# Kernel optimization log

Measured on AMD Instinct MI355X. Metric: run time of the kernel, lower is better.

## Reference

```python
import jax, jax.numpy as jnp
import numpy as np

E = 800000
N = 50000
D = 128
SLOPE = 0.2


def setup_inputs() -> dict:
    key = jax.random.key(0)
    ks = jax.random.split(key, 8)
    M = jax.random.normal(ks[0], (E, D), dtype=jnp.float32)
    dest = jax.random.randint(ks[1], (E,), 0, N, dtype=jnp.int32)
    rev_index = jax.random.randint(ks[2], (E,), 0, E, dtype=jnp.int32)
    s = 1.0 / np.sqrt(D)
    W0 = jax.random.uniform(ks[3], (D, D), jnp.float32, -s, s)
    b0 = jax.random.uniform(ks[4], (D,), jnp.float32, -s, s)
    W1 = jax.random.uniform(ks[5], (D, D), jnp.float32, -s, s)
    b1 = jax.random.uniform(ks[6], (D,), jnp.float32, -s, s)
    sa = 1.0 / np.sqrt(D)
    a_w = jax.random.uniform(ks[7], (1, D), jnp.float32, -sa, sa)
    a_b = jnp.zeros((1,), jnp.float32)
    return {"M": M, "dest": dest, "rev_index": rev_index, "dim_size": N,
            "W0": W0, "b0": b0, "W1": W1, "b1": b1, "a_w": a_w, "a_b": a_b}


def reference(M, dest, rev_index, dim_size, W0, b0, W1, b1, a_w, a_b):
    # Z = LeakyReLU(W_0(M) + W_1(M[rev_index]))  -> [E, D]
    Z = jax.nn.leaky_relu(M @ W0.T + b0 + M[rev_index] @ W1.T + b1, negative_slope=SLOPE)
    # scores = a(Z) -> [E, 1]; segment softmax over dest
    s = (Z @ a_w.T + a_b)[:, 0]  # [E]
    smax = jax.ops.segment_max(s, dest, num_segments=dim_size)  # [N]
    e = jnp.exp(s - smax[dest])
    denom = jax.ops.segment_sum(e, dest, num_segments=dim_size)  # [N]
    alpha = (e / denom[dest])[:, None]  # [E, 1]
    out = jax.ops.segment_sum(alpha * M, dest, num_segments=dim_size)  # [N, D]
    return out, alpha
```

## Files before the change

kernel.cpp:

```cpp
#include <hip/hip_runtime.h>
#include <hip/hip_bf16.h>


#define SLOPE 0.2f
constexpr int E = 800000;
constexpr int N = 50000;
constexpr int D = 128;
constexpr int TILE_E = 64;
constexpr int NTILES = E / TILE_E;
constexpr int LDA = 264;
constexpr int MAXDEG = 64;

typedef __attribute__((ext_vector_type(8))) short bf16x8;
typedef __attribute__((ext_vector_type(4))) short short4v;
typedef __attribute__((ext_vector_type(4))) float f32x4;

__device__ __forceinline__ short f2bf(float f) {
    unsigned u = __float_as_uint(f);
    u = (u + 0x7fffu + ((u >> 16) & 1u)) >> 16;
    return (short)u;
}

__global__ void convert_w(const float* __restrict__ W0, const float* __restrict__ W1,
                          short* __restrict__ Wbf) {
    int i = blockIdx.x * blockDim.x + threadIdx.x;
    if (i >= D * 256) return;
    int d = i >> 8, k = i & 255;
    float v = (k < 128) ? W0[d * 128 + k] : W1[d * 128 + (k - 128)];
    Wbf[i] = f2bf(v);
}

__global__ void bucket_build(const int* __restrict__ dest, int* __restrict__ cnt,
                             int* __restrict__ bucket) {
    int e = blockIdx.x * blockDim.x + threadIdx.x;
    if (e >= E) return;
    int n = dest[e];
    int pos = atomicAdd(&cnt[n], 1);
    if (pos < MAXDEG) bucket[n * MAXDEG + pos] = e;
}

__global__ __launch_bounds__(512) void score_kernel(
    const float* __restrict__ M, const int* __restrict__ dest,
    const int* __restrict__ rev, const short* __restrict__ Wbf,
    const float* __restrict__ b0, const float* __restrict__ b1,
    const float* __restrict__ a_w, const float* __restrict__ a_b,
    float* __restrict__ pbuf, float* __restrict__ denom)
{
    __shared__ short Alds[TILE_E * LDA];
    __shared__ float red[4][TILE_E];

    const int t = threadIdx.x;
    const int w = t >> 6;
    const int lane = t & 63;
    const int lo = lane & 15, hi = lane >> 4;
    const int er = (w & 1) * 32;
    const int dr = (w >> 1) * 32;

    bf16x8 b[2][8];
#pragma unroll
    for (int j = 0; j < 2; ++j) {
        int d = dr + j * 16 + lo;
#pragma unroll
        for (int ks = 0; ks < 8; ++ks)
            b[j][ks] = *(const bf16x8*)(Wbf + d * 256 + ks * 32 + hi * 8);
    }
    float bs[2], aw[2];
#pragma unroll
    for (int j = 0; j < 2; ++j) {
        int d = dr + j * 16 + lo;
        bs[j] = b0[d] + b1[d];
        aw[j] = a_w[d];
    }
    const float ab = a_b[0];

    const int c  = t & 31;
    const int r0 = t >> 5;

    for (int tile = blockIdx.x; tile < NTILES; tile += gridDim.x) {
        const int ebase = tile * TILE_E;
        __syncthreads();

#pragma unroll
        for (int pp = 0; pp < 2; ++pp) {
            float4 vs[2], vr[2];
            int rv[2];
#pragma unroll
            for (int q = 0; q < 2; ++q)
                rv[q] = rev[ebase + r0 + (pp * 2 + q) * 16];
#pragma unroll
            for (int q = 0; q < 2; ++q)
                vs[q] = ((const float4*)(M + (size_t)(ebase + r0 + (pp * 2 + q) * 16) * D))[c];
#pragma unroll
            for (int q = 0; q < 2; ++q)
                vr[q] = ((const float4*)(M + (size_t)rv[q] * D))[c];
#pragma unroll
            for (int q = 0; q < 2; ++q) {
                int r = r0 + (pp * 2 + q) * 16;
                short4v s0 = { f2bf(vs[q].x), f2bf(vs[q].y), f2bf(vs[q].z), f2bf(vs[q].w) };
                *(short4v*)(Alds + r * LDA + c * 4) = s0;
                short4v s1 = { f2bf(vr[q].x), f2bf(vr[q].y), f2bf(vr[q].z), f2bf(vr[q].w) };
                *(short4v*)(Alds + r * LDA + 128 + c * 4) = s1;
            }
        }
        __syncthreads();

        f32x4 zero = {0.f, 0.f, 0.f, 0.f};
        f32x4 acc[2][2];
#pragma unroll
        for (int i = 0; i < 2; ++i)
#pragma unroll
            for (int j = 0; j < 2; ++j) acc[i][j] = zero;

#pragma unroll
        for (int ks = 0; ks < 8; ++ks) {
            bf16x8 a[2];
#pragma unroll
            for (int i = 0; i < 2; ++i)
                a[i] = *(const bf16x8*)(Alds + (er + i * 16 + lo) * LDA + ks * 32 + hi * 8);
#pragma unroll
            for (int i = 0; i < 2; ++i)
#pragma unroll
                for (int j = 0; j < 2; ++j)
                    acc[i][j] = __builtin_amdgcn_mfma_f32_16x16x32_bf16(a[i], b[j][ks], acc[i][j], 0, 0, 0);
        }

#pragma unroll
        for (int i = 0; i < 2; ++i) {
#pragma unroll
            for (int r = 0; r < 4; ++r) {
                float v = 0.f;
#pragma unroll
                for (int j = 0; j < 2; ++j) {
                    float x = acc[i][j][r] + bs[j];
                    x = (x > 0.f) ? x : SLOPE * x;
                    v += aw[j] * x;
                }
                v += __shfl_xor(v, 1);
                v += __shfl_xor(v, 2);
                v += __shfl_xor(v, 4);
                v += __shfl_xor(v, 8);
                if (lo == 0) red[w >> 1][er + i * 16 + hi * 4 + r] = v;
            }
        }
        __syncthreads();

        if (t < TILE_E) {
            float s = red[0][t] + red[1][t] + red[2][t] + red[3][t] + ab;
            float p = __expf(s);
            pbuf[ebase + t] = p;
            atomicAdd(&denom[dest[ebase + t]], p);
        }
    }
}

__global__ void norm_kernel(const int* __restrict__ dest, const float* __restrict__ denom,
                            float* __restrict__ alpha) {
    int e = blockIdx.x * blockDim.x + threadIdx.x;
    if (e < E) alpha[e] = alpha[e] / denom[dest[e]];
}

__global__ __launch_bounds__(256) void gather_kernel(
    const float* __restrict__ M, const float* __restrict__ alpha,
    const int* __restrict__ cnt, const int* __restrict__ bucket,
    float* __restrict__ out)
{
    const int n = blockIdx.x * 4 + (threadIdx.x >> 6);
    const int lane = threadIdx.x & 63;
    int c = cnt[n];
    c = (c > MAXDEG) ? MAXDEG : c;
    int e = 0; float a = 0.f;
    if (lane < c) {
        e = bucket[n * MAXDEG + lane];
        a = alpha[e];
    }
    float2 acc = {0.f, 0.f};
    for (int i = 0; i < c; ++i) {
        int   ei = __shfl(e, i);
        float ai = __shfl(a, i);
        float2 v = ((const float2*)(M + (size_t)ei * D))[lane];
        acc.x += ai * v.x;
        acc.y += ai * v.y;
    }
    ((float2*)(out + (size_t)n * D))[lane] = acc;
}

extern "C" void kernel_launch(void* const* d_in, const int* in_sizes, int n_in,
                              void* d_out, int out_size, void* d_ws, size_t ws_size,
                              hipStream_t stream) {
    const float* M   = (const float*)d_in[0];
    const int*   dst = (const int*)d_in[1];
    const int*   rev = (const int*)d_in[2];
    const float* W0  = (const float*)d_in[4];
    const float* b0  = (const float*)d_in[5];
    const float* W1  = (const float*)d_in[6];
    const float* b1  = (const float*)d_in[7];
    const float* a_w = (const float*)d_in[8];
    const float* a_b = (const float*)d_in[9];

    float* out   = (float*)d_out;
    float* alpha = out + (size_t)N * D;

    float* denom  = (float*)d_ws;
    short* Wbf    = (short*)(denom + N);
    int*   cnt    = (int*)(Wbf + D * 256);
    int*   bucket = cnt + N;

    hipMemsetAsync(denom, 0, (size_t)N * sizeof(float), stream);
    hipMemsetAsync(cnt, 0, (size_t)N * sizeof(int), stream);

    convert_w<<<128, 256, 0, stream>>>(W0, W1, Wbf);
    bucket_build<<<(E + 255) / 256, 256, 0, stream>>>(dst, cnt, bucket);
    score_kernel<<<512, 512, 0, stream>>>(M, dst, rev, Wbf, b0, b1, a_w, a_b, alpha, denom);
    norm_kernel<<<(E + 255) / 256, 256, 0, stream>>>(dst, denom, alpha);
    gather_kernel<<<N / 4, 256, 0, stream>>>(M, alpha, cnt, bucket, out);
}
```

Baseline: 766.3 us.

## Pre-convert M to bf16 and stream tiles into LDS via direct global loads

Adds a pass that converts M to a bf16 copy once. The score kernel then loads that copy straight into a swizzled LDS layout with global_load_lds, and the gather kernel also reads the bf16 copy. The normalisation kernel is folded into the gather, which now writes alpha itself. The intent is to shrink the memory traffic of the later passes and drop one launch, at the cost of an extra full read-and-write pass over M. The output aggregation also loses precision because it now sums bf16 values of M.

```diff
diff --git a/kernel.cpp b/kernel.cpp
--- a/kernel.cpp
+++ b/kernel.cpp
@@ -8,26 +8,38 @@
 constexpr int D = 128;
 constexpr int TILE_E = 64;
 constexpr int NTILES = E / TILE_E;
-constexpr int LDA = 264;
 constexpr int MAXDEG = 64;
 
 typedef __attribute__((ext_vector_type(8))) short bf16x8;
-typedef __attribute__((ext_vector_type(4))) short short4v;
+typedef __attribute__((ext_vector_type(8))) unsigned short u16x8;
 typedef __attribute__((ext_vector_type(4))) float f32x4;
 
-__device__ __forceinline__ short f2bf(float f) {
+__device__ __forceinline__ unsigned short f2bf(float f) {
     unsigned u = __float_as_uint(f);
     u = (u + 0x7fffu + ((u >> 16) & 1u)) >> 16;
-    return (short)u;
+    return (unsigned short)u;
 }
 
 __global__ void convert_w(const float* __restrict__ W0, const float* __restrict__ W1,
-                          short* __restrict__ Wbf) {
+                          unsigned short* __restrict__ Wbf) {
     int i = blockIdx.x * blockDim.x + threadIdx.x;
     if (i >= D * 256) return;
     int d = i >> 8, k = i & 255;
     float v = (k < 128) ? W0[d * 128 + k] : W1[d * 128 + (k - 128)];
     Wbf[i] = f2bf(v);
+}
+
+__global__ void convert_m(const float* __restrict__ M, unsigned short* __restrict__ Mbf) {
+    const size_t nchunk = (size_t)E * D / 8;
+    const size_t stride = (size_t)gridDim.x * blockDim.x;
+    for (size_t i = (size_t)blockIdx.x * blockDim.x + threadIdx.x; i < nchunk; i += stride) {
+        float4 v0 = ((const float4*)M)[i * 2];
+        float4 v1 = ((const float4*)M)[i * 2 + 1];
+        u16x8 u;
+        u[0] = f2bf(v0.x); u[1] = f2bf(v0.y); u[2] = f2bf(v0.z); u[3] = f2bf(v0.w);
+        u[4] = f2bf(v1.x); u[5] = f2bf(v1.y); u[6] = f2bf(v1.z); u[7] = f2bf(v1.w);
+        ((u16x8*)Mbf)[i] = u;
+    }
 }
 
 __global__ void bucket_build(const int* __restrict__ dest, int* __restrict__ cnt,
@@ -39,14 +51,14 @@
     if (pos < MAXDEG) bucket[n * MAXDEG + pos] = e;
 }
 
-__global__ __launch_bounds__(512) void score_kernel(
-    const float* __restrict__ M, const int* __restrict__ dest,
-    const int* __restrict__ rev, const short* __restrict__ Wbf,
+__global__ __launch_bounds__(512, 4) void score_kernel(
+    const unsigned short* __restrict__ Mbf, const int* __restrict__ dest,
+    const int* __restrict__ rev, const unsigned short* __restrict__ Wbf,
     const float* __restrict__ b0, const float* __restrict__ b1,
     const float* __restrict__ a_w, const float* __restrict__ a_b,
     float* __restrict__ pbuf, float* __restrict__ denom)
 {
-    __shared__ short Alds[TILE_E * LDA];
+    __shared__ unsigned short Alds[TILE_E * 256];
     __shared__ float red[4][TILE_E];
 
     const int t = threadIdx.x;
@@ -73,34 +85,29 @@
     }
     const float ab = a_b[0];
 
-    const int c  = t & 31;
-    const int r0 = t >> 5;
+    const int rbase = w * 8;
+    const int rsub = lane >> 5;
+    const int pc = lane & 31;
 
     for (int tile = blockIdx.x; tile < NTILES; tile += gridDim.x) {
         const int ebase = tile * TILE_E;
         __syncthreads();
 
-#pragma unroll
-        for (int pp = 0; pp < 2; ++pp) {
-            float4 vs[2], vr[2];
-            int rv[2];
-#pragma unroll
-            for (int q = 0; q < 2; ++q)
-                rv[q] = rev[ebase + r0 + (pp * 2 + q) * 16];
-#pragma unroll
-            for (int q = 0; q < 2; ++q)
-                vs[q] = ((const float4*)(M + (size_t)(ebase + r0 + (pp * 2 + q) * 16) * D))[c];
-#pragma unroll
-            for (int q = 0; q < 2; ++q)
-                vr[q] = ((const float4*)(M + (size_t)rv[q] * D))[c];
-#pragma unroll
-            for (int q = 0; q < 2; ++q) {
-                int r = r0 + (pp * 2 + q) * 16;
-                short4v s0 = { f2bf(vs[q].x), f2bf(vs[q].y), f2bf(vs[q].z), f2bf(vs[q].w) };
-                *(short4v*)(Alds + r * LDA + c * 4) = s0;
-                short4v s1 = { f2bf(vr[q].x), f2bf(vr[q].y), f2bf(vr[q].z), f2bf(vr[q].w) };
-                *(short4v*)(Alds + r * LDA + 128 + c * 4) = s1;
-            }
+        int revr[4];
+#pragma unroll
+        for (int k = 0; k < 4; ++k)
+            revr[k] = rev[ebase + rbase + 2 * k + rsub];
+#pragma unroll
+        for (int k = 0; k < 4; ++k) {
+            int r = rbase + 2 * k + rsub;
+            int cc = pc ^ (r & 7);
+            const unsigned short* g = (cc < 16)
+                ? Mbf + (size_t)(ebase + r) * 128 + cc * 8
+                : Mbf + (size_t)revr[k] * 128 + (cc - 16) * 8;
+            __builtin_amdgcn_global_load_lds(
+                (const __attribute__((address_space(1))) void*)g,
+                (__attribute__((address_space(3))) void*)(&Alds[(rbase + 2 * k) * 256]),
+                16, 0, 0);
         }
         __syncthreads();
 
@@ -115,8 +122,11 @@
         for (int ks = 0; ks < 8; ++ks) {
             bf16x8 a[2];
 #pragma unroll
-            for (int i = 0; i < 2; ++i)
-                a[i] = *(const bf16x8*)(Alds + (er + i * 16 + lo) * LDA + ks * 32 + hi * 8);
+            for (int i = 0; i < 2; ++i) {
+                int r = er + i * 16 + lo;
+                int pcx = (ks * 4 + hi) ^ (r & 7);
+                a[i] = *(const bf16x8*)(&Alds[r * 256 + pcx * 8]);
+            }
 #pragma unroll
             for (int i = 0; i < 2; ++i)
 #pragma unroll
@@ -153,33 +163,32 @@
     }
 }
 
-__global__ void norm_kernel(const int* __restrict__ dest, const float* __restrict__ denom,
-                            float* __restrict__ alpha) {
-    int e = blockIdx.x * blockDim.x + threadIdx.x;
-    if (e < E) alpha[e] = alpha[e] / denom[dest[e]];
-}
-
 __global__ __launch_bounds__(256) void gather_kernel(
-    const float* __restrict__ M, const float* __restrict__ alpha,
-    const int* __restrict__ cnt, const int* __restrict__ bucket,
-    float* __restrict__ out)
+    const unsigned short* __restrict__ Mbf, const float* __restrict__ p,
+    const float* __restrict__ denom, const int* __restrict__ cnt,
+    const int* __restrict__ bucket, float* __restrict__ out,
+    float* __restrict__ alpha_out)
 {
     const int n = blockIdx.x * 4 + (threadIdx.x >> 6);
     const int lane = threadIdx.x & 63;
     int c = cnt[n];
     c = (c > MAXDEG) ? MAXDEG : c;
+    float dn = denom[n];
     int e = 0; float a = 0.f;
     if (lane < c) {
         e = bucket[n * MAXDEG + lane];
-        a = alpha[e];
+        a = p[e] / dn;
+        alpha_out[e] = a;
     }
     float2 acc = {0.f, 0.f};
     for (int i = 0; i < c; ++i) {
         int   ei = __shfl(e, i);
         float ai = __shfl(a, i);
-        float2 v = ((const float2*)(M + (size_t)ei * D))[lane];
-        acc.x += ai * v.x;
-        acc.y += ai * v.y;
+        unsigned v = *(const unsigned*)(Mbf + (size_t)ei * 128 + lane * 2);
+        float f0 = __uint_as_float((v & 0x0000ffffu) << 16);
+        float f1 = __uint_as_float(v & 0xffff0000u);
+        acc.x += ai * f0;
+        acc.y += ai * f1;
     }
     ((float2*)(out + (size_t)n * D))[lane] = acc;
 }
@@ -200,17 +209,19 @@
     float* out   = (float*)d_out;
     float* alpha = out + (size_t)N * D;
 
-    float* denom  = (float*)d_ws;
-    short* Wbf    = (short*)(denom + N);
-    int*   cnt    = (int*)(Wbf + D * 256);
-    int*   bucket = cnt + N;
+    float*          denom  = (float*)d_ws;
+    unsigned short* Wbf    = (unsigned short*)(denom + N);
+    int*            cnt    = (int*)(Wbf + D * 256);
+    int*            bucket = cnt + N;
+    float*          pbuf   = (float*)(bucket + (size_t)N * MAXDEG);
+    unsigned short* Mbf    = (unsigned short*)(pbuf + E);
 
     hipMemsetAsync(denom, 0, (size_t)N * sizeof(float), stream);
     hipMemsetAsync(cnt, 0, (size_t)N * sizeof(int), stream);
 
     convert_w<<<128, 256, 0, stream>>>(W0, W1, Wbf);
+    convert_m<<<8192, 256, 0, stream>>>(M, Mbf);
     bucket_build<<<(E + 255) / 256, 256, 0, stream>>>(dst, cnt, bucket);
-    score_kernel<<<512, 512, 0, stream>>>(M, dst, rev, Wbf, b0, b1, a_w, a_b, alpha, denom);
-    norm_kernel<<<(E + 255) / 256, 256, 0, stream>>>(dst, denom, alpha);
-    gather_kernel<<<N / 4, 256, 0, stream>>>(M, alpha, cnt, bucket, out);
-}
+    score_kernel<<<512, 512, 0, stream>>>(Mbf, dst, rev, Wbf, b0, b1, a_w, a_b, pbuf, denom);
+    gather_kernel<<<N / 4, 256, 0, stream>>>(Mbf, pbuf, denom, cnt, bucket, out, alpha);
+}
```

New measurement: 828.1 us. 1.08x slower.
